# Kernel tuning notes

Hardware: AMD Instinct MI355X
Metric: run time of the kernel (lower is better)

## Reference

```python
import jax, jax.numpy as jnp
import numpy as np

D = 384; NH = 4; FF = 1024; NL = 2
L_ENC = 750; T_AUD = 1500; VOCAB = 60; T_TXT = 256; B = 8; S_SPK = 8; GAMA = 1.0


def _conv1d(x, w, b, stride):
    y = jax.lax.conv_general_dilated(x, w, (stride,), [(1, 1)], dimension_numbers=("NCH", "OIH", "NCH"))
    return y + b[None, :, None]


def _ln(x, g, b):
    m = x.mean(-1, keepdims=True)
    v = ((x - m) ** 2).mean(-1, keepdims=True)
    return (x - m) * jax.lax.rsqrt(v + 1e-5) * g + b


def _enc_layer(x, qkv_w, qkv_b, ow, ob, f1w, f1b, f2w, f2b, g1, b1, g2, b2):
    Bq, L, d = x.shape
    hd = d // NH
    q, k, v = jnp.split(x @ qkv_w.T + qkv_b, 3, axis=-1)
    q = q.reshape(Bq, L, NH, hd); k = k.reshape(Bq, L, NH, hd); v = v.reshape(Bq, L, NH, hd)
    s = jnp.einsum("blhd,bmhd->bhlm", q, k) * np.float32(1.0 / np.sqrt(hd))
    a = jax.nn.softmax(s, axis=-1)
    ctx = jnp.einsum("bhlm,bmhd->blhd", a, v).reshape(Bq, L, d)
    x = _ln(x + ctx @ ow.T + ob, g1, b1)
    h = jax.nn.relu(x @ f1w.T + f1b) @ f2w.T + f2b
    return _ln(x + h, g2, b2)


def _gru(x, h, wih, whh, bih, bhh):
    gi = x @ wih.T + bih
    gh = h @ whh.T + bhh
    ir, iz, inn = jnp.split(gi, 3, axis=-1)
    hr, hz, hn = jnp.split(gh, 3, axis=-1)
    r = jax.nn.sigmoid(ir + hr)
    z = jax.nn.sigmoid(iz + hz)
    n = jnp.tanh(inn + r * hn)
    return (1.0 - z) * n + z * h


def _nll(logits, tgt):
    # torch F.nll_loss applied to raw scores (faithful to source), ignore_index=-100
    valid = (tgt != -100)
    idx = jnp.where(valid, tgt, 0)
    picked = jnp.take_along_axis(logits, idx[..., None], axis=-1)[..., 0]
    return -(picked * valid).sum() / jnp.maximum(valid.sum(), 1).astype(logits.dtype)


def _forward(fl, target_asr_ids, target_diar_ids, remat=False):
    (input_features, speaker_inventory, conv1_w, conv1_b, conv2_w, conv2_b,
     asr_qkv_w, asr_qkv_b, asr_attn_out_w, asr_attn_out_b, asr_ff1_w, asr_ff1_b,
     asr_ff2_w, asr_ff2_b, asr_ln1_g, asr_ln1_b, asr_ln2_g, asr_ln2_b,
     diar_qkv_w, diar_qkv_b, diar_attn_out_w, diar_attn_out_b, diar_ff1_w, diar_ff1_b,
     diar_ff2_w, diar_ff2_b, diar_ln1_g, diar_ln1_b, diar_ln2_g, diar_ln2_b,
     la_q_w, la_k_w, la_v_w, la_in_b, la_out_w, la_out_b, emb,
     asr_rnn_w_ih, asr_rnn_w_hh, asr_rnn_b_ih, asr_rnn_b_hh,
     diar_rnn_w_ih, diar_rnn_w_hh, diar_rnn_b_ih, diar_rnn_b_hh,
     asr_out_w, asr_out_b, d2a_w, d2a_b, h2a_w, h2a_b) = fl
    x = jax.nn.relu(_conv1d(input_features, conv1_w, conv1_b, 1))
    x = jax.nn.relu(_conv1d(x, conv2_w, conv2_b, 2))
    x = jnp.transpose(x, (0, 2, 1))  # [B, L_ENC, D]
    enc_asr = x
    for l in range(NL):
        enc_asr = _enc_layer(enc_asr, asr_qkv_w[l], asr_qkv_b[l], asr_attn_out_w[l], asr_attn_out_b[l],
                             asr_ff1_w[l], asr_ff1_b[l], asr_ff2_w[l], asr_ff2_b[l],
                             asr_ln1_g[l], asr_ln1_b[l], asr_ln2_g[l], asr_ln2_b[l])
    enc_diar = x
    for l in range(NL):
        enc_diar = _enc_layer(enc_diar, diar_qkv_w[l], diar_qkv_b[l], diar_attn_out_w[l], diar_attn_out_b[l],
                              diar_ff1_w[l], diar_ff1_b[l], diar_ff2_w[l], diar_ff2_b[l],
                              diar_ln1_g[l], diar_ln1_b[l], diar_ln2_g[l], diar_ln2_b[l])
    Bsz = x.shape[0]
    inv_norm = jnp.linalg.norm(speaker_inventory, axis=2)  # [B, S]

    def step(carry, tgt):
        token, asr_ctx, h_asr, h_diar, attns = carry
        e = emb[token]  # [B, D]
        h_asr = _gru(jnp.concatenate([asr_ctx, e], 1), h_asr,
                     asr_rnn_w_ih, asr_rnn_w_hh, asr_rnn_b_ih, asr_rnn_b_hh)
        # 1-dim MultiheadAttention: q=h_asr[:,:,None], k=prev attentions, v=enc_asr (vdim=384->1)
        q = h_asr[:, :, None] * la_q_w[0, 0] + la_in_b[0]   # [B, L, 1]
        k = attns * la_k_w[0, 0] + la_in_b[1]               # [B, L, 1]
        v = enc_asr @ la_v_w.T + la_in_b[2]                 # [B, L, 1]
        s = q @ jnp.swapaxes(k, 1, 2)                       # [B, L, L]; head_dim=1 -> scale 1
        a = jax.nn.softmax(s, axis=-1)
        attns_new = (a @ v) * la_out_w[0, 0] + la_out_b[0]  # [B, L, 1]
        w = attns_new[..., 0]
        asr_ctx_new = jnp.einsum("bld,bl->bd", enc_asr, w)
        spk_ctx = jnp.einsum("bld,bl->bd", enc_diar, w)
        h_diar_new = _gru(jnp.concatenate([spk_ctx, e], 1), h_diar,
                          diar_rnn_w_ih, diar_rnn_w_hh, diar_rnn_b_ih, diar_rnn_b_hh)
        sc = jnp.einsum("bsd,bd->bs", speaker_inventory, h_diar_new)
        hn = jnp.linalg.norm(h_diar_new, axis=1, keepdims=True)
        beta = jax.nn.softmax(sc / (hn * inv_norm), axis=1)
        spk_state = jnp.einsum("bsd,bs->bd", speaker_inventory, beta)
        logits = (asr_ctx_new + h_asr @ h2a_w.T + h2a_b + spk_state @ d2a_w.T + d2a_b) @ asr_out_w.T + asr_out_b
        next_tok = jnp.where(tgt == -100, 0, tgt)
        return (next_tok, asr_ctx_new, h_asr, h_diar_new, attns_new), (logits, beta)

    step_fn = jax.checkpoint(step) if remat else step
    init = (jnp.zeros((Bsz,), jnp.int32),
            jnp.zeros((Bsz, D), jnp.float32),
            jnp.zeros((Bsz, L_ENC), jnp.float32),
            jnp.zeros((Bsz, D), jnp.float32),
            jnp.zeros((Bsz, L_ENC, 1), jnp.float32))
    _, (logits_seq, beta_seq) = jax.lax.scan(step_fn, init, jnp.swapaxes(target_asr_ids, 0, 1))
    asr_outputs = jnp.swapaxes(logits_seq, 0, 1)   # [B, T, VOCAB]
    diar_outputs = jnp.swapaxes(beta_seq, 0, 1)    # [B, T, S]
    loss = _nll(asr_outputs, target_asr_ids) + GAMA * _nll(diar_outputs, target_diar_ids)
    return asr_outputs, diar_outputs, loss


def setup_inputs() -> dict:
    key = jax.random.key(0)
    cnt = [0]
    def p(shape, scale=0.05):
        cnt[0] += 1
        return jax.random.normal(jax.random.fold_in(key, cnt[0]), shape, dtype=jnp.float32) * scale
    inp = {}
    inp["input_features"] = p((B, 80, T_AUD), 1.0)
    inp["speaker_inventory"] = p((B, S_SPK, D), 1.0)
    inp["conv1_w"] = p((D, 80, 3)); inp["conv1_b"] = p((D,))
    inp["conv2_w"] = p((D, D, 3)); inp["conv2_b"] = p((D,))
    for pre in ("asr", "diar"):
        inp[pre + "_qkv_w"] = p((NL, 3 * D, D)); inp[pre + "_qkv_b"] = p((NL, 3 * D))
        inp[pre + "_attn_out_w"] = p((NL, D, D)); inp[pre + "_attn_out_b"] = p((NL, D))
        inp[pre + "_ff1_w"] = p((NL, FF, D)); inp[pre + "_ff1_b"] = p((NL, FF))
        inp[pre + "_ff2_w"] = p((NL, D, FF)); inp[pre + "_ff2_b"] = p((NL, D))
        inp[pre + "_ln1_g"] = jnp.ones((NL, D), jnp.float32); inp[pre + "_ln1_b"] = jnp.zeros((NL, D), jnp.float32)
        inp[pre + "_ln2_g"] = jnp.ones((NL, D), jnp.float32); inp[pre + "_ln2_b"] = jnp.zeros((NL, D), jnp.float32)
    inp["la_q_w"] = p((1, 1), 1.0); inp["la_k_w"] = p((1, 1), 1.0); inp["la_v_w"] = p((1, D))
    inp["la_in_b"] = p((3,)); inp["la_out_w"] = p((1, 1), 1.0); inp["la_out_b"] = p((1,))
    inp["emb"] = p((VOCAB, D), 1.0)
    inp["asr_rnn_w_ih"] = p((3 * L_ENC, 2 * D)); inp["asr_rnn_w_hh"] = p((3 * L_ENC, L_ENC))
    inp["asr_rnn_b_ih"] = p((3 * L_ENC,)); inp["asr_rnn_b_hh"] = p((3 * L_ENC,))
    inp["diar_rnn_w_ih"] = p((3 * D, 2 * D)); inp["diar_rnn_w_hh"] = p((3 * D, D))
    inp["diar_rnn_b_ih"] = p((3 * D,)); inp["diar_rnn_b_hh"] = p((3 * D,))
    inp["asr_out_w"] = p((VOCAB, D)); inp["asr_out_b"] = p((VOCAB,))
    inp["d2a_w"] = p((D, D)); inp["d2a_b"] = p((D,))
    inp["h2a_w"] = p((D, L_ENC)); inp["h2a_b"] = p((D,))
    inp["target_asr_ids"] = jax.random.randint(jax.random.fold_in(key, 9001), (B, T_TXT), 0, VOCAB, dtype=jnp.int32)
    inp["target_diar_ids"] = jax.random.randint(jax.random.fold_in(key, 9002), (B, T_TXT), 0, S_SPK, dtype=jnp.int32)
    return inp


def reference(input_features, speaker_inventory, conv1_w, conv1_b, conv2_w, conv2_b,
              asr_qkv_w, asr_qkv_b, asr_attn_out_w, asr_attn_out_b, asr_ff1_w, asr_ff1_b,
              asr_ff2_w, asr_ff2_b, asr_ln1_g, asr_ln1_b, asr_ln2_g, asr_ln2_b,
              diar_qkv_w, diar_qkv_b, diar_attn_out_w, diar_attn_out_b, diar_ff1_w, diar_ff1_b,
              diar_ff2_w, diar_ff2_b, diar_ln1_g, diar_ln1_b, diar_ln2_g, diar_ln2_b,
              la_q_w, la_k_w, la_v_w, la_in_b, la_out_w, la_out_b, emb,
              asr_rnn_w_ih, asr_rnn_w_hh, asr_rnn_b_ih, asr_rnn_b_hh,
              diar_rnn_w_ih, diar_rnn_w_hh, diar_rnn_b_ih, diar_rnn_b_hh,
              asr_out_w, asr_out_b, d2a_w, d2a_b, h2a_w, h2a_b,
              target_asr_ids, target_diar_ids):
    fl = (input_features, speaker_inventory, conv1_w, conv1_b, conv2_w, conv2_b,
          asr_qkv_w, asr_qkv_b, asr_attn_out_w, asr_attn_out_b, asr_ff1_w, asr_ff1_b,
          asr_ff2_w, asr_ff2_b, asr_ln1_g, asr_ln1_b, asr_ln2_g, asr_ln2_b,
          diar_qkv_w, diar_qkv_b, diar_attn_out_w, diar_attn_out_b, diar_ff1_w, diar_ff1_b,
          diar_ff2_w, diar_ff2_b, diar_ln1_g, diar_ln1_b, diar_ln2_g, diar_ln2_b,
          la_q_w, la_k_w, la_v_w, la_in_b, la_out_w, la_out_b, emb,
          asr_rnn_w_ih, asr_rnn_w_hh, asr_rnn_b_ih, asr_rnn_b_hh,
          diar_rnn_w_ih, diar_rnn_w_hh, diar_rnn_b_ih, diar_rnn_b_hh,
          asr_out_w, asr_out_b, d2a_w, d2a_b, h2a_w, h2a_b)
    return _forward(fl, target_asr_ids, target_diar_ids, remat=False)
```

## Files before the change

kernel.cpp:

```cpp
#include <hip/hip_runtime.h>
#include <math.h>

#define L_ENC 750
#define T_AUD 1500
#define DD    384
#define FF    1024
#define NHH   4
#define HDIM  96
#define VOCAB 60
#define T_TXT 256
#define BB    8
#define NB    240
#define TB    512

static __device__ __forceinline__ float sigmf(float x){ return 1.f/(1.f + __expf(-x)); }

static __device__ __forceinline__ float cld(const float* p){
  return __hip_atomic_load(p, __ATOMIC_RELAXED, __HIP_MEMORY_SCOPE_AGENT);
}
static __device__ __forceinline__ void cst(float* p, float v){
  __hip_atomic_store(p, v, __ATOMIC_RELAXED, __HIP_MEMORY_SCOPE_AGENT);
}

static constexpr size_t O_X  = 0;
static constexpr size_t O_EA = 2304000;
static constexpr size_t O_ED = 4608000;
static constexpr size_t O_ST = 6912000;
static constexpr size_t oHASR = O_ST + 0;
static constexpr size_t oATT0 = O_ST + 6000;
static constexpr size_t oATT1 = O_ST + 12000;
static constexpr size_t oHD   = O_ST + 18000;
static constexpr size_t oACTX = O_ST + 21072;
static constexpr size_t oSCTX = O_ST + 27216;
static constexpr size_t oPREP = O_ST + 33360;
static constexpr size_t oGIA  = O_ST + 39504;
static constexpr size_t oGHA  = O_ST + 57504;
static constexpr size_t oGID  = O_ST + 75504;
static constexpr size_t oGHD  = O_ST + 84720;
static constexpr size_t oLACC = O_ST + 93936;
static constexpr size_t oVLA  = O_ST + 93944;
static constexpr size_t oINVN = O_ST + 99944;
static constexpr size_t oBAR  = O_ST + 100008;
static constexpr size_t oZ384 = O_ST + 102100;
static constexpr size_t O_SCR = O_ST + 103000;
static constexpr size_t oWIHAT_A = O_SCR + 0;
static constexpr size_t oWHHT_A  = O_SCR + 864000;
static constexpr size_t oWIHAT_D = O_SCR + 2556000;
static constexpr size_t oWHHT_D  = O_SCR + 2998368;
static constexpr size_t oH2AT    = O_SCR + 3440736;
static constexpr size_t oAOT     = O_SCR + 3728736;
static constexpr size_t oEMBT    = O_SCR + 3751776;
static constexpr size_t oGEA     = O_SCR + 4538208;
static constexpr size_t oGED     = O_SCR + 9146208;
static constexpr size_t oDIB     = O_SCR + 11505504;

__global__ void transpose_k(const float* __restrict__ in, int ldin, int R, int C,
                            float* __restrict__ out){
  __shared__ float t[32][33];
  int c0 = blockIdx.x*32, r0 = blockIdx.y*32;
  int x = threadIdx.x, y = threadIdx.y;
  for (int i = y; i < 32; i += 8){
    int r = r0 + i, c = c0 + x;
    t[i][x] = (r < R && c < C) ? in[(size_t)r*ldin + c] : 0.f;
  }
  __syncthreads();
  for (int i = y; i < 32; i += 8){
    int c = c0 + i, r = r0 + x;
    if (c < C && r < R) out[(size_t)c*R + r] = t[x][i];
  }
}

__global__ void packT_k(const float* __restrict__ in, int ldin, int R, int K,
                        float* __restrict__ out){
  __shared__ float tl[32][33];
  int k0 = blockIdx.x*32, r0 = blockIdx.y*32;
  int x = threadIdx.x, y = threadIdx.y;
  int K4 = ((K + 3) >> 2) << 2;
  for (int i = y; i < 32; i += 8){
    int r = r0 + i, k = k0 + x;
    tl[i][x] = (r < R && k < K) ? in[(size_t)r*ldin + k] : 0.f;
  }
  __syncthreads();
  for (int i = y; i < 32; i += 8){
    int k = k0 + i, r = r0 + x;
    if (k < K4 && r < R) out[((size_t)(k >> 2)*R + r)*4 + (k & 3)] = tl[x][i];
  }
}

__global__ void kt_k(const float* __restrict__ QKV, float* __restrict__ KT){
  __shared__ float t[32][33];
  int z = blockIdx.z; int b = z >> 2, h = z & 3;
  const float* in = QKV + (size_t)b*L_ENC*1152 + 384 + h*HDIM;
  float* out = KT + (size_t)z*HDIM*L_ENC;
  int c0 = blockIdx.x*32, r0 = blockIdx.y*32;
  int x = threadIdx.x, y = threadIdx.y;
  for (int i = y; i < 32; i += 8){
    int r = r0 + i, c = c0 + x;
    t[i][x] = (r < L_ENC && c < HDIM) ? in[(size_t)r*1152 + c] : 0.f;
  }
  __syncthreads();
  for (int i = y; i < 32; i += 8){
    int c = c0 + i, r = r0 + x;
    if (c < HDIM && r < L_ENC) out[(size_t)c*L_ENC + r] = t[x][i];
  }
}

template<int RELU, int HASRES>
__global__ __launch_bounds__(256) void gemm_k(
    const float* __restrict__ A, int lda, const float* __restrict__ W, int ldw,
    const float* __restrict__ bias, const float* __restrict__ Res,
    float* __restrict__ C, int ldc, int M, int N, int K)
{
  __shared__ __align__(16) float As[16][132];
  __shared__ __align__(16) float Ws[16][68];
  int tid = threadIdx.x;
  int row0 = blockIdx.y*128, col0 = blockIdx.x*64;
  int tx = tid & 15, ty = tid >> 4;
  int lr = tid >> 2, lk = (tid & 3)*4;
  float acc[8][4] = {};
  for (int k0 = 0; k0 < K; k0 += 16){
    float4 a0 = make_float4(0,0,0,0), a1 = make_float4(0,0,0,0), w0 = make_float4(0,0,0,0);
    int r0i = row0 + lr, r1i = row0 + 64 + lr, wri = col0 + lr;
    if (r0i < M) a0 = *(const float4*)(A + (size_t)r0i*lda + k0 + lk);
    if (r1i < M) a1 = *(const float4*)(A + (size_t)r1i*lda + k0 + lk);
    if (wri < N) w0 = *(const float4*)(W + (size_t)wri*ldw + k0 + lk);
    As[lk+0][lr] = a0.x; As[lk+1][lr] = a0.y; As[lk+2][lr] = a0.z; As[lk+3][lr] = a0.w;
    As[lk+0][64+lr] = a1.x; As[lk+1][64+lr] = a1.y; As[lk+2][64+lr] = a1.z; As[lk+3][64+lr] = a1.w;
    Ws[lk+0][lr] = w0.x; Ws[lk+1][lr] = w0.y; Ws[lk+2][lr] = w0.z; Ws[lk+3][lr] = w0.w;
    __syncthreads();
    #pragma unroll
    for (int k = 0; k < 16; k++){
      float4 b4 = *(const float4*)&Ws[k][tx*4];
      float4 a4 = *(const float4*)&As[k][ty*8];
      float4 a5 = *(const float4*)&As[k][ty*8+4];
      acc[0][0] += a4.x*b4.x; acc[0][1] += a4.x*b4.y; acc[0][2] += a4.x*b4.z; acc[0][3] += a4.x*b4.w;
      acc[1][0] += a4.y*b4.x; acc[1][1] += a4.y*b4.y; acc[1][2] += a4.y*b4.z; acc[1][3] += a4.y*b4.w;
      acc[2][0] += a4.z*b4.x; acc[2][1] += a4.z*b4.y; acc[2][2] += a4.z*b4.z; acc[2][3] += a4.z*b4.w;
      acc[3][0] += a4.w*b4.x; acc[3][1] += a4.w*b4.y; acc[3][2] += a4.w*b4.z; acc[3][3] += a4.w*b4.w;
      acc[4][0] += a5.x*b4.x; acc[4][1] += a5.x*b4.y; acc[4][2] += a5.x*b4.z; acc[4][3] += a5.x*b4.w;
      acc[5][0] += a5.y*b4.x; acc[5][1] += a5.y*b4.y; acc[5][2] += a5.y*b4.z; acc[5][3] += a5.y*b4.w;
      acc[6][0] += a5.z*b4.x; acc[6][1] += a5.z*b4.y; acc[6][2] += a5.z*b4.z; acc[6][3] += a5.z*b4.w;
      acc[7][0] += a5.w*b4.x; acc[7][1] += a5.w*b4.y; acc[7][2] += a5.w*b4.z; acc[7][3] += a5.w*b4.w;
    }
    __syncthreads();
  }
  #pragma unroll
  for (int ii = 0; ii < 8; ii++){
    int m = row0 + ty*8 + ii;
    if (m >= M) continue;
    #pragma unroll
    for (int jj = 0; jj < 4; jj++){
      int n = col0 + tx*4 + jj;
      if (n >= N) continue;
      float v = acc[ii][jj] + bias[n];
      if (HASRES) v += Res[(size_t)m*ldc + n];
      if (RELU) v = fmaxf(v, 0.f);
      C[(size_t)m*ldc + n] = v;
    }
  }
}

__global__ void im2col1(const float* __restrict__ in, float* __restrict__ P){
  int t = blockIdx.x, b = blockIdx.y, i = threadIdx.x;
  if (i >= 240) return;
  int ic = i/3, kt = i - ic*3;
  int p = t + kt - 1;
  P[((size_t)(b*T_AUD + t))*240 + i] = (p >= 0 && p < T_AUD) ? in[((size_t)(b*80 + ic))*T_AUD + p] : 0.f;
}

__global__ __launch_bounds__(384) void im2col2(const float* __restrict__ X1T, float* __restrict__ P){
  int t = blockIdx.x, b = blockIdx.y, ic = threadIdx.x;
  size_t ob = ((size_t)(b*L_ENC + t))*1152 + (size_t)ic*3;
  #pragma unroll
  for (int kt = 0; kt < 3; kt++){
    int p = 2*t + kt - 1;
    P[ob + kt] = (p >= 0 && p < T_AUD) ? X1T[((size_t)(b*T_AUD + p))*DD + ic] : 0.f;
  }
}

__global__ __launch_bounds__(256) void dup_k(const float* __restrict__ src,
    float* __restrict__ a, float* __restrict__ b){
  size_t i = (size_t)blockIdx.x*256 + threadIdx.x;
  float4 v = ((const float4*)src)[i];
  ((float4*)a)[i] = v;
  ((float4*)b)[i] = v;
}

__global__ __launch_bounds__(128) void ln_k(float* __restrict__ X, const float* __restrict__ g,
                                            const float* __restrict__ bt){
  int r = blockIdx.x, tid = threadIdx.x;
  float* p = X + (size_t)r*DD;
  float v0 = p[tid], v1 = p[tid+128], v2 = p[tid+256];
  __shared__ float red[128];
  red[tid] = v0+v1+v2; __syncthreads();
  for (int k = 64; k > 0; k >>= 1){ if (tid < k) red[tid] += red[tid+k]; __syncthreads(); }
  float m = red[0] * (1.f/384.f);
  __syncthreads();
  float d0 = v0-m, d1 = v1-m, d2 = v2-m;
  red[tid] = d0*d0 + d1*d1 + d2*d2; __syncthreads();
  for (int k = 64; k > 0; k >>= 1){ if (tid < k) red[tid] += red[tid+k]; __syncthreads(); }
  float rs = rsqrtf(red[0]*(1.f/384.f) + 1e-5f);
  p[tid]     = d0*rs*g[tid]     + bt[tid];
  p[tid+128] = d1*rs*g[tid+128] + bt[tid+128];
  p[tid+256] = d2*rs*g[tid+256] + bt[tid+256];
}

__global__ __launch_bounds__(1024) void attn_enc(const float* __restrict__ QKV,
    const float* __restrict__ KT, float* __restrict__ ctx){
  int b = blockIdx.z, h = blockIdx.y, i0 = blockIdx.x*16;
  int tid = threadIdx.x, lane = tid & 63, wv = tid >> 6;
  __shared__ float q_s[16][96];
  __shared__ float p_s[16][752];
  __shared__ float den_s[16];
  for (int idx = tid; idx < 16*96; idx += 1024){
    int r2 = idx/96, c = idx - r2*96; int i = i0 + r2;
    q_s[r2][c] = (i < L_ENC) ? QKV[((size_t)(b*L_ENC + i))*1152 + h*HDIM + c]*0.10206207f : 0.f;
  }
  __syncthreads();
  int i = i0 + wv;
  const float* ktb = KT + ((size_t)(b*4 + h))*HDIM*L_ENC;
  if (i < L_ENC){
    float sr[12] = {0,0,0,0,0,0,0,0,0,0,0,0};
    for (int c = 0; c < 96; c++){
      float qc = q_s[wv][c];
      const float* kr = ktb + c*L_ENC + lane;
      #pragma unroll
      for (int jt = 0; jt < 12; jt++) sr[jt] += qc*kr[jt*64];
    }
    float mx = -1e30f;
    #pragma unroll
    for (int jt = 0; jt < 12; jt++){ if (lane + jt*64 < L_ENC) mx = fmaxf(mx, sr[jt]); }
    #pragma unroll
    for (int o = 32; o > 0; o >>= 1) mx = fmaxf(mx, __shfl_xor(mx, o));
    float den = 0.f;
    #pragma unroll
    for (int jt = 0; jt < 12; jt++){
      int j = lane + jt*64;
      if (j < L_ENC){ float e = __expf(sr[jt]-mx); p_s[wv][j] = e; den += e; }
    }
    #pragma unroll
    for (int o = 32; o > 0; o >>= 1) den += __shfl_xor(den, o);
    if (lane == 0) den_s[wv] = den;
  }
  __syncthreads();
  if (i < L_ENC){
    float idn = 1.f/den_s[wv];
    const float* vb = QKV + (size_t)b*L_ENC*1152 + 768 + h*HDIM;
    float a0 = 0.f, a1 = 0.f;
    for (int j = 0; j < L_ENC; j++){
      float pj = p_s[wv][j];
      const float* vr = vb + (size_t)j*1152;
      a0 += pj*vr[lane];
      if (lane < 32) a1 += pj*vr[lane + 64];
    }
    size_t ob = ((size_t)(b*L_ENC + i))*DD + h*HDIM;
    ctx[ob + lane] = a0*idn;
    if (lane < 32) ctx[ob + lane + 64] = a1*idn;
  }
}

__global__ __launch_bounds__(384) void embed_k(const float* __restrict__ emb,
    const int* __restrict__ tgtA, float* __restrict__ E){
  int row = blockIdx.x; int t = row >> 3, b = row & 7;
  int tok = 0;
  if (t > 0){ int v = tgtA[b*T_TXT + t - 1]; tok = (v == -100) ? 0 : v; }
  E[(size_t)row*DD + threadIdx.x] = emb[(size_t)tok*DD + threadIdx.x];
}

__global__ __launch_bounds__(256) void vla_k(const float* __restrict__ EA,
    const float* __restrict__ lav, const float* __restrict__ lain, float* __restrict__ VLA){
  int row = blockIdx.x*4 + (threadIdx.x >> 6);
  int lane = threadIdx.x & 63;
  if (row >= BB*L_ENC) return;
  const float* p = EA + (size_t)row*DD;
  float s = 0.f;
  for (int d = lane; d < DD; d += 64) s += p[d]*lav[d];
  #pragma unroll
  for (int o = 32; o > 0; o >>= 1) s += __shfl_xor(s, o);
  if (lane == 0) VLA[row] = s + lain[2];
}

__global__ void invn_k(const float* __restrict__ inv, float* __restrict__ INVN){
  int row = blockIdx.x; int lane = threadIdx.x;
  float s = 0.f;
  for (int d = lane; d < DD; d += 64){ float v = inv[(size_t)row*DD + d]; s += v*v; }
  #pragma unroll
  for (int o = 32; o > 0; o >>= 1) s += __shfl_xor(s, o);
  if (lane == 0) INVN[row] = sqrtf(s);
}

struct DecParams {
  float* ws; float* out;
  const float* ABHH; const float* DBHH;
  const float* SPK;  const float* AOB;
  const float* LAQ; const float* LAK; const float* LAIB; const float* LAOW; const float* LAOB;
  const float* H2AB; const float* D2AB;
  const int* TGTA; const int* TGTD;
};

static __device__ __forceinline__ void gbar(unsigned* s, unsigned epoch){
  __syncthreads();
  int tid = threadIdx.x;
  if (blockIdx.x == 0){
    if (tid > 0 && tid < NB){
      while (__hip_atomic_load(&s[tid*4], __ATOMIC_RELAXED, __HIP_MEMORY_SCOPE_AGENT) < epoch)
        __builtin_amdgcn_s_sleep(4);
    }
    __syncthreads();
    if (tid < NB)
      __hip_atomic_store(&s[(256 + tid)*4], epoch, __ATOMIC_RELAXED, __HIP_MEMORY_SCOPE_AGENT);
  } else {
    if (tid == 0){
      __hip_atomic_store(&s[blockIdx.x*4], epoch, __ATOMIC_RELAXED, __HIP_MEMORY_SCOPE_AGENT);
      while (__hip_atomic_load(&s[(256 + blockIdx.x)*4], __ATOMIC_RELAXED, __HIP_MEMORY_SCOPE_AGENT) < epoch)
        __builtin_amdgcn_s_sleep(4);
    }
    __syncthreads();
  }
}

#define FMA8(acc, s_, base) { const float4 b0_ = *(const float4*)&(base)[0]; const float4 b1_ = *(const float4*)&(base)[4]; \
  acc[0]+=b0_.x*(s_); acc[1]+=b0_.y*(s_); acc[2]+=b0_.z*(s_); acc[3]+=b0_.w*(s_); \
  acc[4]+=b1_.x*(s_); acc[5]+=b1_.y*(s_); acc[6]+=b1_.z*(s_); acc[7]+=b1_.w*(s_); }

template<int NR, int KH, int KQH>
__device__ void gates_fn(int task, const float* __restrict__ WIT, const float* __restrict__ WHT,
                         const float* __restrict__ ctxv, const float* __restrict__ hv,
                         const float* __restrict__ GE, const float* __restrict__ bhh,
                         float* __restrict__ GI, float* __restrict__ GH, int t, float* SM)
{
  constexpr int CHQ = (KQH + 31) / 32;
  float* ac  = SM;
  float* hh  = SM + 3072;
  float* pgi = SM + 3072 + KQH*32;
  float* pgh = pgi + 4096;
  int tid = threadIdx.x;
  for (int idx = tid; idx < 3072; idx += TB){ int b = idx/384, k = idx - b*384; ac[k*8+b] = cld(&ctxv[idx]); }
  for (int idx = tid; idx < KH*8;  idx += TB){ int b = idx/KH,  k = idx - b*KH;  hh[k*8+b] = cld(&hv[idx]); }
  for (int idx = KH*8 + tid; idx < KQH*32; idx += TB) hh[idx] = 0.f;
  __syncthreads();
  int rl = tid & 15, kp = tid >> 4;
  int r = task*16 + rl;
  float gi[8] = {}, gh[8] = {};
  if (r < NR){
    const float4* W4 = (const float4*)WIT;
    int q0 = kp*3;
    #pragma unroll
    for (int q = q0; q < q0+3; q++){
      float4 w4 = W4[(size_t)q*NR + r];
      const float* a = &ac[q*32];
      FMA8(gi, w4.x, a+0); FMA8(gi, w4.y, a+8); FMA8(gi, w4.z, a+16); FMA8(gi, w4.w, a+24);
    }
    const float4* WH4 = (const float4*)WHT;
    int h0 = kp*CHQ, h1 = (h0 + CHQ < KQH) ? h0 + CHQ : KQH;
    for (int q = h0; q < h1; q++){
      float4 w4 = WH4[(size_t)q*NR + r];
      const float* a = &hh[q*32];
      FMA8(gh, w4.x, a+0); FMA8(gh, w4.y, a+8); FMA8(gh, w4.z, a+16); FMA8(gh, w4.w, a+24);
    }
  }
  #pragma unroll
  for (int b = 0; b < 8; b++){ pgi[(kp*16+rl)*8 + b] = gi[b]; pgh[(kp*16+rl)*8 + b] = gh[b]; }
  __syncthreads();
  if (tid < 16){
    int rr = task*16 + tid;
    if (rr < NR){
      #pragma unroll
      for (int b = 0; b < 8; b++){
        float s1 = 0.f, s2 = 0.f;
        for (int kq = 0; kq < 32; kq++){ s1 += pgi[(kq*16+tid)*8 + b]; s2 += pgh[(kq*16+tid)*8 + b]; }
        cst(&GI[(size_t)b*NR + rr], s1 + GE[((size_t)t*8 + b)*NR + rr]);
        cst(&GH[(size_t)b*NR + rr], s2 + bhh[rr]);
      }
    }
  }
  __syncthreads();
}

__device__ void phase_hattn_ctx(int bid, int t, float* ws, const DecParams& P, float* SM)
{
  float* kk = SM;
  float* vv = SM + 768;
  float* wl = SM + 1536;
  float* hl = SM + 1568;
  float* part = SM + 1600;
  int tid = threadIdx.x;
  int b = bid & 7, chunk = bid >> 3;
  int i0 = chunk*26; int n = L_ENC - i0; if (n > 26) n = 26;
  const float* acur = ws + ((t & 1) ? oATT1 : oATT0);
  float*       anxt = ws + ((t & 1) ? oATT0 : oATT1);
  const float* GIAp = ws + oGIA; const float* GHAp = ws + oGHA;
  float* HASRp = ws + oHASR;
  const float* VLAp = ws + oVLA;
  float kw = P.LAK[0], kb = P.LAIB[1];
  for (int j = tid; j < L_ENC; j += TB){
    kk[j] = cld(&acur[b*L_ENC + j])*kw + kb;
    vv[j] = VLAp[b*L_ENC + j];
  }
  __syncthreads();
  int wv = tid >> 6, lane = tid & 63;
  float laq = P.LAQ[0], li0 = P.LAIB[0], low = P.LAOW[0], lob = P.LAOB[0];
  for (int il = wv; il < n; il += 8){
    int i = i0 + il;
    int base = b*2250 + i;
    float rr = sigmf(cld(&GIAp[base]) + cld(&GHAp[base]));
    float zz = sigmf(cld(&GIAp[base+750]) + cld(&GHAp[base+750]));
    float nn = tanhf(cld(&GIAp[base+1500]) + rr*cld(&GHAp[base+1500]));
    float h = (1.f - zz)*nn + zz*cld(&HASRp[b*L_ENC + i]);
    float q = h*laq + li0;
    float sr[12]; float mx = -1e30f;
    #pragma unroll
    for (int jt = 0; jt < 12; jt++){
      int j = lane + jt*64;
      float s = (j < L_ENC) ? q*kk[j] : -1e30f;
      sr[jt] = s; mx = fmaxf(mx, s);
    }
    #pragma unroll
    for (int o = 32; o > 0; o >>= 1) mx = fmaxf(mx, __shfl_xor(mx, o));
    float se = 0.f, sv = 0.f;
    #pragma unroll
    for (int jt = 0; jt < 12; jt++){
      int j = lane + jt*64;
      if (j < L_ENC){ float e = __expf(sr[jt] - mx); se += e; sv += e*vv[j]; }
    }
    #pragma unroll
    for (int o = 32; o > 0; o >>= 1){ se += __shfl_xor(se, o); sv += __shfl_xor(sv, o); }
    if (lane == 0){
      cst(&HASRp[b*L_ENC + i], h);
      float w = (sv/se)*low + lob;
      cst(&anxt[b*L_ENC + i], w);
      wl[il] = w; hl[il] = h;
    }
  }
  __syncthreads();
  if (tid < 480){
    int lg = tid / 96, dq = tid - lg*96;
    int d0 = dq*4;
    const float* EAb = ws + O_EA + (size_t)b*L_ENC*DD + d0;
    const float* EDb = ws + O_ED + (size_t)b*L_ENC*DD + d0;
    const float* H2b = ws + oH2AT + d0;
    float4 a4 = {0,0,0,0}, s4 = {0,0,0,0}, h4 = {0,0,0,0};
    for (int j = lg; j < n; j += 5){
      size_t lo = (size_t)(i0 + j)*DD;
      float wj = wl[j], hj = hl[j];
      float4 e = *(const float4*)(EAb + lo);
      a4.x += e.x*wj; a4.y += e.y*wj; a4.z += e.z*wj; a4.w += e.w*wj;
      float4 e2 = *(const float4*)(EDb + lo);
      s4.x += e2.x*wj; s4.y += e2.y*wj; s4.z += e2.z*wj; s4.w += e2.w*wj;
      float4 e3 = *(const float4*)(H2b + lo);
      h4.x += e3.x*hj; h4.y += e3.y*hj; h4.z += e3.z*hj; h4.w += e3.w*hj;
    }
    float* pp = part + (size_t)tid*12;
    *(float4*)pp = a4; *(float4*)(pp+4) = s4; *(float4*)(pp+8) = h4;
  }
  __syncthreads();
  if (tid < 96){
    float4 ra = {0,0,0,0}, rs = {0,0,0,0}, rh = {0,0,0,0};
    #pragma unroll
    for (int g = 0; g < 5; g++){
      const float* pp = part + (size_t)(g*96 + tid)*12;
      float4 pa = *(const float4*)pp, ps = *(const float4*)(pp+4), ph = *(const float4*)(pp+8);
      ra.x += pa.x; ra.y += pa.y; ra.z += pa.z; ra.w += pa.w;
      rs.x += ps.x; rs.y += ps.y; rs.z += ps.z; rs.w += ps.w;
      rh.x += ph.x; rh.y += ph.y; rh.z += ph.z; rh.w += ph.w;
    }
    int par = t & 1;
    int d0 = tid*4;
    float* A = &ws[oACTX + par*3072 + b*DD + d0];
    float* S = &ws[oSCTX + par*3072 + b*DD + d0];
    float* Pr = &ws[oPREP + par*3072 + b*DD + d0];
    atomicAdd(&A[0], ra.x); atomicAdd(&A[1], ra.y); atomicAdd(&A[2], ra.z); atomicAdd(&A[3], ra.w);
    atomicAdd(&S[0], rs.x); atomicAdd(&S[1], rs.y); atomicAdd(&S[2], rs.z); atomicAdd(&S[3], rs.w);
    atomicAdd(&Pr[0], ra.x+rh.x); atomicAdd(&Pr[1], ra.y+rh.y);
    atomicAdd(&Pr[2], ra.z+rh.z); atomicAdd(&Pr[3], ra.w+rh.w);
  }
  __syncthreads();
}

__device__ void phase_final(int b, int t, float* ws, const float* prep,
                            const DecParams& P, float* SM)
{
  float* hd_s = SM;
  float* pre_s = SM + 384;
  float* red = SM + 768;
  float* beta_s = SM + 1280;
  float* sc_s = SM + 1288;
  float* part2 = SM + 1296;
  int tid = threadIdx.x;
  bool act = tid < DD;
  const float* GIDp = ws + oGID; const float* GHDp = ws + oGHD;
  float* HDp = ws + oHD;
  float h = 0.f;
  if (act){
    int base = b*1152 + tid;
    float rr = sigmf(cld(&GIDp[base]) + cld(&GHDp[base]));
    float zz = sigmf(cld(&GIDp[base+384]) + cld(&GHDp[base+384]));
    float nn = tanhf(cld(&GIDp[base+768]) + rr*cld(&GHDp[base+768]));
    h = (1.f - zz)*nn + zz*cld(&HDp[b*DD + tid]);
    hd_s[tid] = h; cst(&HDp[b*DD + tid], h);
  }
  red[tid] = act ? h*h : 0.f;
  __syncthreads();
  for (int s = 256; s > 0; s >>= 1){ if (tid < s) red[tid] += red[tid+s]; __syncthreads(); }
  float hn = sqrtf(red[0]);
  int sg = tid >> 6, lane = tid & 63;
  float ps = 0.f;
  for (int j = lane; j < DD; j += 64) ps += P.SPK[((size_t)(b*8 + sg))*DD + j]*hd_s[j];
  #pragma unroll
  for (int o = 32; o > 0; o >>= 1) ps += __shfl_xor(ps, o);
  if (lane == 0) sc_s[sg] = ps / (hn * ws[oINVN + b*8 + sg]);
  __syncthreads();
  if (tid == 0){
    float mx = -1e30f;
    for (int s2 = 0; s2 < 8; s2++) mx = fmaxf(mx, sc_s[s2]);
    float sm = 0.f;
    for (int s2 = 0; s2 < 8; s2++){ float e = __expf(sc_s[s2] - mx); beta_s[s2] = e; sm += e; }
    float isv = 1.f/sm;
    for (int s2 = 0; s2 < 8; s2++) beta_s[s2] *= isv;
    int td = P.TGTD[b*T_TXT + t];
    if (td != -100){ atomicAdd(&ws[oLACC+2], beta_s[td]); atomicAdd(&ws[oLACC+3], 1.f); }
  }
  __syncthreads();
  if (tid < 8) P.out[122880 + ((size_t)(b*T_TXT + t))*8 + tid] = beta_s[tid];
  if (act){
    float p = cld(&prep[b*DD + tid]);
    const float* Mb = ws + oDIB + (size_t)(b*8)*DD + tid;
    #pragma unroll
    for (int s2 = 0; s2 < 8; s2++) p += beta_s[s2]*Mb[(size_t)s2*DD];
    pre_s[tid] = p;
  }
  __syncthreads();
  {
    int vg = tid >> 6, v = tid & 63;
    float pl = 0.f;
    if (v < VOCAB){
      const float* AOTp = ws + oAOT;
      int d0 = vg*48;
      for (int d2 = d0; d2 < d0+48; d2++) pl += pre_s[d2]*AOTp[d2*VOCAB + v];
    }
    part2[vg*64 + v] = pl;
  }
  __syncthreads();
  if (tid < VOCAB){
    float lg = P.AOB[tid];
    #pragma unroll
    for (int g = 0; g < 8; g++) lg += part2[g*64 + tid];
    P.out[((size_t)(b*T_TXT + t))*VOCAB + tid] = lg;
    int ta = P.TGTA[b*T_TXT + t];
    if (ta == tid) atomicAdd(&ws[oLACC+0], lg);
    if (tid == 0 && ta != -100) atomicAdd(&ws[oLACC+1], 1.f);
  }
  __syncthreads();
}

__global__ __launch_bounds__(TB) void dec_loop(DecParams P)
{
  __shared__ __align__(16) float SM[17280];
  int bid = blockIdx.x;
  float* ws = P.ws;
  unsigned* slots = (unsigned*)(ws + oBAR);
  unsigned ep = 0;

  if (bid < 141)
    gates_fn<2250,750,188>(bid, ws+oWIHAT_A, ws+oWHHT_A, ws+oACTX, ws+oHASR,
                           ws+oGEA, P.ABHH, ws+oGIA, ws+oGHA, 0, SM);
  else if (bid < 149){
    int b = bid - 141;
    for (int d = threadIdx.x; d < DD; d += TB)
      cst(&ws[oPREP + b*DD + d], P.H2AB[d] + P.D2AB[d]);
  }
  gbar(slots, ++ep);

  for (int t = 0; t <= T_TXT; t++){
    if (t < T_TXT && bid < 232) phase_hattn_ctx(bid, t, ws, P, SM);
    else if (bid >= 232 && t >= 1)
      phase_final(bid - 232, t - 1, ws, ws + oPREP + ((t-1) & 1)*3072, P, SM);
    gbar(slots, ++ep);
    if (t == T_TXT) break;

    if (bid < 72)
      gates_fn<1152,384,96>(bid, ws+oWIHAT_D, ws+oWHHT_D, ws+oSCTX+(t&1)*3072, ws+oHD,
                            ws+oGED, P.DBHH, ws+oGID, ws+oGHD, t, SM);
    else if (bid < 213){
      if (t + 1 < T_TXT)
        gates_fn<2250,750,188>(bid-72, ws+oWIHAT_A, ws+oWHHT_A, ws+oACTX+(t&1)*3072, ws+oHASR,
                               ws+oGEA, P.ABHH, ws+oGIA, ws+oGHA, t+1, SM);
    } else if (bid < 221 && t + 1 < T_TXT){
      int b = bid - 213, par = (t + 1) & 1;
      for (int d = threadIdx.x; d < DD; d += TB){
        cst(&ws[oACTX + par*3072 + b*DD + d], 0.f);
        cst(&ws[oSCTX + par*3072 + b*DD + d], 0.f);
        cst(&ws[oPREP + par*3072 + b*DD + d], P.H2AB[d] + P.D2AB[d]);
      }
    }
    gbar(slots, ++ep);
  }
}

__global__ void loss_final_k(const float* __restrict__ lacc, float* __restrict__ out){
  if (threadIdx.x == 0 && blockIdx.x == 0){
    float la = lacc[0]/fmaxf(lacc[1], 1.f);
    float ld = lacc[2]/fmaxf(lacc[3], 1.f);
    out[139264] = -(la + ld);
  }
}

extern "C" void kernel_launch(void* const* d_in, const int* in_sizes, int n_in,
                              void* d_out, int out_size, void* d_ws, size_t ws_size,
                              hipStream_t stream)
{
  (void)in_sizes; (void)n_in; (void)out_size; (void)ws_size;
  float* ws  = (float*)d_ws;
  float* out = (float*)d_out;

  const float* IN0   = (const float*)d_in[0];
  const float* SPK   = (const float*)d_in[1];
  const float* C1W   = (const float*)d_in[2];
  const float* C1B   = (const float*)d_in[3];
  const float* C2W   = (const float*)d_in[4];
  const float* C2B   = (const float*)d_in[5];
  const float* LAQ   = (const float*)d_in[30];
  const float* LAK   = (const float*)d_in[31];
  const float* LAV   = (const float*)d_in[32];
  const float* LAIB  = (const float*)d_in[33];
  const float* LAOW  = (const float*)d_in[34];
  const float* LAOB  = (const float*)d_in[35];
  const float* EMB   = (const float*)d_in[36];
  const float* AWIH  = (const float*)d_in[37];
  const float* AWHH  = (const float*)d_in[38];
  const float* ABIH  = (const float*)d_in[39];
  const float* ABHH  = (const float*)d_in[40];
  const float* DWIH  = (const float*)d_in[41];
  const float* DWHH  = (const float*)d_in[42];
  const float* DBIH  = (const float*)d_in[43];
  const float* DBHH  = (const float*)d_in[44];
  const float* AOW   = (const float*)d_in[45];
  const float* AOB   = (const float*)d_in[46];
  const float* D2AW  = (const float*)d_in[47];
  const float* D2AB  = (const float*)d_in[48];
  const float* H2AW  = (const float*)d_in[49];
  const float* H2AB  = (const float*)d_in[50];
  const int*   TGTA  = (const int*)d_in[51];
  const int*   TGTD  = (const int*)d_in[52];

  const size_t S_QKV = O_SCR;
  const size_t S_KT  = O_SCR + 6912000;
  const size_t S_CTX = O_SCR + 9216000;
  const size_t S_Y   = O_SCR + 11520000;
  const size_t S_H   = O_SCR + 13824000;
  const size_t X1T   = S_KT;
  const size_t Pc1   = S_H;
  const size_t Pc2   = S_QKV;

  hipMemsetAsync((void*)(ws + O_ST), 0, 103000*sizeof(float), stream);

  im2col1<<<dim3(1500,8), 256, 0, stream>>>(IN0, ws + Pc1);
  gemm_k<1,0><<<dim3(6,94), 256, 0, stream>>>(ws+Pc1, 240, C1W, 240, C1B, nullptr, ws+X1T, 384, 12000, 384, 240);
  im2col2<<<dim3(750,8), 384, 0, stream>>>(ws+X1T, ws+Pc2);
  gemm_k<1,0><<<dim3(6,47), 256, 0, stream>>>(ws+Pc2, 1152, C2W, 1152, C2B, nullptr, ws+O_X, 384, 6000, 384, 1152);

  dup_k<<<2250, 256, 0, stream>>>(ws+O_X, ws+O_EA, ws+O_ED);

  auto enc_layer = [&](float* Xb, const float* qw, const float* qb, const float* ow,
                       const float* ob, const float* f1w, const float* f1b,
                       const float* f2w, const float* f2b,
                       const float* g1, const float* b1, const float* g2, const float* b2){
    gemm_k<0,0><<<dim3(18,47), 256, 0, stream>>>(Xb, 384, qw, 384, qb, nullptr, ws+S_QKV, 1152, 6000, 1152, 384);
    kt_k<<<dim3(3,24,32), dim3(32,8), 0, stream>>>(ws+S_QKV, ws+S_KT);
    attn_enc<<<dim3(47,4,8), 1024, 0, stream>>>(ws+S_QKV, ws+S_KT, ws+S_CTX);
    gemm_k<0,1><<<dim3(6,47), 256, 0, stream>>>(ws+S_CTX, 384, ow, 384, ob, Xb, ws+S_Y, 384, 6000, 384, 384);
    ln_k<<<6000, 128, 0, stream>>>(ws+S_Y, g1, b1);
    gemm_k<1,0><<<dim3(16,47), 256, 0, stream>>>(ws+S_Y, 384, f1w, 384, f1b, nullptr, ws+S_H, 1024, 6000, 1024, 384);
    gemm_k<0,1><<<dim3(6,47), 256, 0, stream>>>(ws+S_H, 1024, f2w, 1024, f2b, ws+S_Y, Xb, 384, 6000, 384, 1024);
    ln_k<<<6000, 128, 0, stream>>>(Xb, g2, b2);
  };
  for (int st = 0; st < 2; st++){
    int base = (st == 0) ? 6 : 18;
    float* Xb = ws + ((st == 0) ? O_EA : O_ED);
    const float* qkvw = (const float*)d_in[base+0];
    const float* qkvb = (const float*)d_in[base+1];
    const float* aow  = (const float*)d_in[base+2];
    const float* aob2 = (const float*)d_in[base+3];
    const float* f1w  = (const float*)d_in[base+4];
    const float* f1b  = (const float*)d_in[base+5];
    const float* f2w  = (const float*)d_in[base+6];
    const float* f2b  = (const float*)d_in[base+7];
    const float* g1   = (const float*)d_in[base+8];
    const float* b1   = (const float*)d_in[base+9];
    const float* g2   = (const float*)d_in[base+10];
    const float* b2   = (const float*)d_in[base+11];
    for (int l = 0; l < 2; l++){
      enc_layer(Xb, qkvw + (size_t)l*1152*384, qkvb + (size_t)l*1152,
                aow + (size_t)l*384*384, aob2 + (size_t)l*384,
                f1w + (size_t)l*1024*384, f1b + (size_t)l*1024,
                f2w + (size_t)l*384*1024, f2b + (size_t)l*384,
                g1 + (size_t)l*384, b1 + (size_t)l*384, g2 + (size_t)l*384, b2 + (size_t)l*384);
    }
  }

  packT_k<<<dim3(12,71), dim3(32,8), 0, stream>>>(AWIH, 768, 2250, 384, ws+oWIHAT_A);
  packT_k<<<dim3(24,71), dim3(32,8), 0, stream>>>(AWHH, 750, 2250, 750, ws+oWHHT_A);
  packT_k<<<dim3(12,36), dim3(32,8), 0, stream>>>(DWIH, 768, 1152, 384, ws+oWIHAT_D);
  packT_k<<<dim3(12,36), dim3(32,8), 0, stream>>>(DWHH, 384, 1152, 384, ws+oWHHT_D);
  transpose_k<<<dim3(24,12), dim3(32,8), 0, stream>>>(H2AW, 750, 384, 750, ws+oH2AT);
  transpose_k<<<dim3(12,2),  dim3(32,8), 0, stream>>>(AOW, 384, 60, 384, ws+oAOT);
  embed_k<<<2048, 384, 0, stream>>>(EMB, TGTA, ws+oEMBT);
  gemm_k<0,0><<<dim3(36,16), 256, 0, stream>>>(ws+oEMBT, 384, AWIH+384, 768, ABIH, nullptr, ws+oGEA, 2250, 2048, 2250, 384);
  gemm_k<0,0><<<dim3(18,16), 256, 0, stream>>>(ws+oEMBT, 384, DWIH+384, 768, DBIH, nullptr, ws+oGED, 1152, 2048, 1152, 384);
  gemm_k<0,0><<<dim3(6,1), 256, 0, stream>>>(SPK, 384, D2AW, 384, ws+oZ384, nullptr, ws+oDIB, 384, 64, 384, 384);
  vla_k<<<1500, 256, 0, stream>>>(ws+O_EA, LAV, LAIB, ws+oVLA);
  invn_k<<<64, 64, 0, stream>>>(SPK, ws+oINVN);

  DecParams DP;
  DP.ws = ws; DP.out = out;
  DP.ABHH = ABHH; DP.DBHH = DBHH; DP.SPK = SPK; DP.AOB = AOB;
  DP.LAQ = LAQ; DP.LAK = LAK; DP.LAIB = LAIB; DP.LAOW = LAOW; DP.LAOB = LAOB;
  DP.H2AB = H2AB; DP.D2AB = D2AB; DP.TGTA = TGTA; DP.TGTD = TGTD;
  dec_loop<<<dim3(NB), dim3(TB), 0, stream>>>(DP);

  loss_final_k<<<1, 64, 0, stream>>>(ws+oLACC, out);
}
```

Before: 20.64 ms.

## Widen GEMM tiles, double decoder grid, parallelize gate reduction

The GEMM kernel now computes 128x128 output tiles with an 8x8 register micro-tile per thread instead of 128x64, halving grid width in every launch and raising arithmetic intensity per shared-memory load. The persistent decoder loop grows from 240 to 480 blocks, with barrier slots and scratch offsets shifted to match, and the gate-partial reduction now splits across 128 threads (row x batch) instead of 16. The GEMM change doubles accumulator registers, which may cut occupancy. Using more decoder blocks spreads the gate matvec K-range thinner but makes each grid barrier more expensive.

```diff
diff --git a/kernel.cpp b/kernel.cpp
--- a/kernel.cpp
+++ b/kernel.cpp
@@ -10,7 +10,7 @@
 #define VOCAB 60
 #define T_TXT 256
 #define BB    8
-#define NB    240
+#define NB    480
 #define TB    512
 
 static __device__ __forceinline__ float sigmf(float x){ return 1.f/(1.f + __expf(-x)); }
@@ -41,8 +41,8 @@
 static constexpr size_t oVLA  = O_ST + 93944;
 static constexpr size_t oINVN = O_ST + 99944;
 static constexpr size_t oBAR  = O_ST + 100008;
-static constexpr size_t oZ384 = O_ST + 102100;
-static constexpr size_t O_SCR = O_ST + 103000;
+static constexpr size_t oZ384 = O_ST + 104200;
+static constexpr size_t O_SCR = O_ST + 105000;
 static constexpr size_t oWIHAT_A = O_SCR + 0;
 static constexpr size_t oWHHT_A  = O_SCR + 864000;
 static constexpr size_t oWIHAT_D = O_SCR + 2556000;
@@ -112,45 +112,51 @@
     float* __restrict__ C, int ldc, int M, int N, int K)
 {
   __shared__ __align__(16) float As[16][132];
-  __shared__ __align__(16) float Ws[16][68];
+  __shared__ __align__(16) float Ws[16][132];
   int tid = threadIdx.x;
-  int row0 = blockIdx.y*128, col0 = blockIdx.x*64;
+  int row0 = blockIdx.y*128, col0 = blockIdx.x*128;
   int tx = tid & 15, ty = tid >> 4;
-  int lr = tid >> 2, lk = (tid & 3)*4;
-  float acc[8][4] = {};
+  int lr = tid >> 1, lk = (tid & 1)*8;
+  float acc[8][8] = {};
+  int ar = row0 + lr, wr = col0 + lr;
   for (int k0 = 0; k0 < K; k0 += 16){
-    float4 a0 = make_float4(0,0,0,0), a1 = make_float4(0,0,0,0), w0 = make_float4(0,0,0,0);
-    int r0i = row0 + lr, r1i = row0 + 64 + lr, wri = col0 + lr;
-    if (r0i < M) a0 = *(const float4*)(A + (size_t)r0i*lda + k0 + lk);
-    if (r1i < M) a1 = *(const float4*)(A + (size_t)r1i*lda + k0 + lk);
-    if (wri < N) w0 = *(const float4*)(W + (size_t)wri*ldw + k0 + lk);
+    float4 a0 = make_float4(0,0,0,0), a1 = make_float4(0,0,0,0);
+    float4 w0 = make_float4(0,0,0,0), w1 = make_float4(0,0,0,0);
+    if (ar < M){
+      const float* ap = A + (size_t)ar*lda + k0 + lk;
+      a0 = *(const float4*)ap; a1 = *(const float4*)(ap + 4);
+    }
+    if (wr < N){
+      const float* wp = W + (size_t)wr*ldw + k0 + lk;
+      w0 = *(const float4*)wp; w1 = *(const float4*)(wp + 4);
+    }
+    __syncthreads();
     As[lk+0][lr] = a0.x; As[lk+1][lr] = a0.y; As[lk+2][lr] = a0.z; As[lk+3][lr] = a0.w;
-    As[lk+0][64+lr] = a1.x; As[lk+1][64+lr] = a1.y; As[lk+2][64+lr] = a1.z; As[lk+3][64+lr] = a1.w;
+    As[lk+4][lr] = a1.x; As[lk+5][lr] = a1.y; As[lk+6][lr] = a1.z; As[lk+7][lr] = a1.w;
     Ws[lk+0][lr] = w0.x; Ws[lk+1][lr] = w0.y; Ws[lk+2][lr] = w0.z; Ws[lk+3][lr] = w0.w;
+    Ws[lk+4][lr] = w1.x; Ws[lk+5][lr] = w1.y; Ws[lk+6][lr] = w1.z; Ws[lk+7][lr] = w1.w;
     __syncthreads();
     #pragma unroll
     for (int k = 0; k < 16; k++){
-      float4 b4 = *(const float4*)&Ws[k][tx*4];
-      float4 a4 = *(const float4*)&As[k][ty*8];
-      float4 a5 = *(const float4*)&As[k][ty*8+4];
-      acc[0][0] += a4.x*b4.x; acc[0][1] += a4.x*b4.y; acc[0][2] += a4.x*b4.z; acc[0][3] += a4.x*b4.w;
-      acc[1][0] += a4.y*b4.x; acc[1][1] += a4.y*b4.y; acc[1][2] += a4.y*b4.z; acc[1][3] += a4.y*b4.w;
-      acc[2][0] += a4.z*b4.x; acc[2][1] += a4.z*b4.y; acc[2][2] += a4.z*b4.z; acc[2][3] += a4.z*b4.w;
-      acc[3][0] += a4.w*b4.x; acc[3][1] += a4.w*b4.y; acc[3][2] += a4.w*b4.z; acc[3][3] += a4.w*b4.w;
-      acc[4][0] += a5.x*b4.x; acc[4][1] += a5.x*b4.y; acc[4][2] += a5.x*b4.z; acc[4][3] += a5.x*b4.w;
-      acc[5][0] += a5.y*b4.x; acc[5][1] += a5.y*b4.y; acc[5][2] += a5.y*b4.z; acc[5][3] += a5.y*b4.w;
-      acc[6][0] += a5.z*b4.x; acc[6][1] += a5.z*b4.y; acc[6][2] += a5.z*b4.z; acc[6][3] += a5.z*b4.w;
-      acc[7][0] += a5.w*b4.x; acc[7][1] += a5.w*b4.y; acc[7][2] += a5.w*b4.z; acc[7][3] += a5.w*b4.w;
-    }
-    __syncthreads();
+      float av[8], bv[8];
+      *(float4*)&av[0] = *(const float4*)&As[k][ty*8];
+      *(float4*)&av[4] = *(const float4*)&As[k][ty*8+4];
+      *(float4*)&bv[0] = *(const float4*)&Ws[k][tx*8];
+      *(float4*)&bv[4] = *(const float4*)&Ws[k][tx*8+4];
+      #pragma unroll
+      for (int ii = 0; ii < 8; ii++){
+        #pragma unroll
+        for (int jj = 0; jj < 8; jj++) acc[ii][jj] += av[ii]*bv[jj];
+      }
+    }
   }
   #pragma unroll
   for (int ii = 0; ii < 8; ii++){
     int m = row0 + ty*8 + ii;
     if (m >= M) continue;
     #pragma unroll
-    for (int jj = 0; jj < 4; jj++){
-      int n = col0 + tx*4 + jj;
+    for (int jj = 0; jj < 8; jj++){
+      int n = col0 + tx*8 + jj;
       if (n >= N) continue;
       float v = acc[ii][jj] + bias[n];
       if (HASRES) v += Res[(size_t)m*ldc + n];
@@ -308,11 +314,11 @@
     }
     __syncthreads();
     if (tid < NB)
-      __hip_atomic_store(&s[(256 + tid)*4], epoch, __ATOMIC_RELAXED, __HIP_MEMORY_SCOPE_AGENT);
+      __hip_atomic_store(&s[(512 + tid)*4], epoch, __ATOMIC_RELAXED, __HIP_MEMORY_SCOPE_AGENT);
   } else {
     if (tid == 0){
       __hip_atomic_store(&s[blockIdx.x*4], epoch, __ATOMIC_RELAXED, __HIP_MEMORY_SCOPE_AGENT);
-      while (__hip_atomic_load(&s[(256 + blockIdx.x)*4], __ATOMIC_RELAXED, __HIP_MEMORY_SCOPE_AGENT) < epoch)
+      while (__hip_atomic_load(&s[(512 + blockIdx.x)*4], __ATOMIC_RELAXED, __HIP_MEMORY_SCOPE_AGENT) < epoch)
         __builtin_amdgcn_s_sleep(4);
     }
     __syncthreads();
@@ -329,7 +335,6 @@
                          const float* __restrict__ GE, const float* __restrict__ bhh,
                          float* __restrict__ GI, float* __restrict__ GH, int t, float* SM)
 {
-  constexpr int CHQ = (KQH + 31) / 32;
   float* ac  = SM;
   float* hh  = SM + 3072;
   float* pgi = SM + 3072 + KQH*32;
@@ -344,15 +349,14 @@
   float gi[8] = {}, gh[8] = {};
   if (r < NR){
     const float4* W4 = (const float4*)WIT;
-    int q0 = kp*3;
-    #pragma unroll
-    for (int q = q0; q < q0+3; q++){
+    int q0 = (kp*96) >> 5, q1 = ((kp+1)*96) >> 5;
+    for (int q = q0; q < q1; q++){
       float4 w4 = W4[(size_t)q*NR + r];
       const float* a = &ac[q*32];
       FMA8(gi, w4.x, a+0); FMA8(gi, w4.y, a+8); FMA8(gi, w4.z, a+16); FMA8(gi, w4.w, a+24);
     }
     const float4* WH4 = (const float4*)WHT;
-    int h0 = kp*CHQ, h1 = (h0 + CHQ < KQH) ? h0 + CHQ : KQH;
+    int h0 = (kp*KQH) >> 5, h1 = ((kp+1)*KQH) >> 5;
     for (int q = h0; q < h1; q++){
       float4 w4 = WH4[(size_t)q*NR + r];
       const float* a = &hh[q*32];
@@ -362,16 +366,15 @@
   #pragma unroll
   for (int b = 0; b < 8; b++){ pgi[(kp*16+rl)*8 + b] = gi[b]; pgh[(kp*16+rl)*8 + b] = gh[b]; }
   __syncthreads();
-  if (tid < 16){
-    int rr = task*16 + tid;
+  if (tid < 128){
+    int rl2 = tid & 15, bb = tid >> 4;
+    int rr = task*16 + rl2;
     if (rr < NR){
+      float s1 = 0.f, s2 = 0.f;
       #pragma unroll
-      for (int b = 0; b < 8; b++){
-        float s1 = 0.f, s2 = 0.f;
-        for (int kq = 0; kq < 32; kq++){ s1 += pgi[(kq*16+tid)*8 + b]; s2 += pgh[(kq*16+tid)*8 + b]; }
-        cst(&GI[(size_t)b*NR + rr], s1 + GE[((size_t)t*8 + b)*NR + rr]);
-        cst(&GH[(size_t)b*NR + rr], s2 + bhh[rr]);
-      }
+      for (int kq = 0; kq < 32; kq++){ s1 += pgi[(kq*16+rl2)*8+bb]; s2 += pgh[(kq*16+rl2)*8+bb]; }
+      cst(&GI[(size_t)bb*NR + rr], s1 + GE[((size_t)t*8 + bb)*NR + rr]);
+      cst(&GH[(size_t)bb*NR + rr], s2 + bhh[rr]);
     }
   }
   __syncthreads();
@@ -553,7 +556,7 @@
   __syncthreads();
 }
 
-__global__ __launch_bounds__(TB) void dec_loop(DecParams P)
+__global__ __launch_bounds__(TB, 4) void dec_loop(DecParams P)
 {
   __shared__ __align__(16) float SM[17280];
   int bid = blockIdx.x;
@@ -573,7 +576,7 @@
 
   for (int t = 0; t <= T_TXT; t++){
     if (t < T_TXT && bid < 232) phase_hattn_ctx(bid, t, ws, P, SM);
-    else if (bid >= 232 && t >= 1)
+    else if (bid >= 232 && bid < 240 && t >= 1)
       phase_final(bid - 232, t - 1, ws, ws + oPREP + ((t-1) & 1)*3072, P, SM);
     gbar(slots, ++ep);
     if (t == T_TXT) break;
@@ -652,12 +655,12 @@
   const size_t Pc1   = S_H;
   const size_t Pc2   = S_QKV;
 
-  hipMemsetAsync((void*)(ws + O_ST), 0, 103000*sizeof(float), stream);
+  hipMemsetAsync((void*)(ws + O_ST), 0, 105000*sizeof(float), stream);
 
   im2col1<<<dim3(1500,8), 256, 0, stream>>>(IN0, ws + Pc1);
-  gemm_k<1,0><<<dim3(6,94), 256, 0, stream>>>(ws+Pc1, 240, C1W, 240, C1B, nullptr, ws+X1T, 384, 12000, 384, 240);
+  gemm_k<1,0><<<dim3(3,94), 256, 0, stream>>>(ws+Pc1, 240, C1W, 240, C1B, nullptr, ws+X1T, 384, 12000, 384, 240);
   im2col2<<<dim3(750,8), 384, 0, stream>>>(ws+X1T, ws+Pc2);
-  gemm_k<1,0><<<dim3(6,47), 256, 0, stream>>>(ws+Pc2, 1152, C2W, 1152, C2B, nullptr, ws+O_X, 384, 6000, 384, 1152);
+  gemm_k<1,0><<<dim3(3,47), 256, 0, stream>>>(ws+Pc2, 1152, C2W, 1152, C2B, nullptr, ws+O_X, 384, 6000, 384, 1152);
 
   dup_k<<<2250, 256, 0, stream>>>(ws+O_X, ws+O_EA, ws+O_ED);
 
@@ -665,13 +668,13 @@
                        const float* ob, const float* f1w, const float* f1b,
                        const float* f2w, const float* f2b,
                        const float* g1, const float* b1, const float* g2, const float* b2){
-    gemm_k<0,0><<<dim3(18,47), 256, 0, stream>>>(Xb, 384, qw, 384, qb, nullptr, ws+S_QKV, 1152, 6000, 1152, 384);
+    gemm_k<0,0><<<dim3(9,47), 256, 0, stream>>>(Xb, 384, qw, 384, qb, nullptr, ws+S_QKV, 1152, 6000, 1152, 384);
     kt_k<<<dim3(3,24,32), dim3(32,8), 0, stream>>>(ws+S_QKV, ws+S_KT);
     attn_enc<<<dim3(47,4,8), 1024, 0, stream>>>(ws+S_QKV, ws+S_KT, ws+S_CTX);
-    gemm_k<0,1><<<dim3(6,47), 256, 0, stream>>>(ws+S_CTX, 384, ow, 384, ob, Xb, ws+S_Y, 384, 6000, 384, 384);
+    gemm_k<0,1><<<dim3(3,47), 256, 0, stream>>>(ws+S_CTX, 384, ow, 384, ob, Xb, ws+S_Y, 384, 6000, 384, 384);
     ln_k<<<6000, 128, 0, stream>>>(ws+S_Y, g1, b1);
-    gemm_k<1,0><<<dim3(16,47), 256, 0, stream>>>(ws+S_Y, 384, f1w, 384, f1b, nullptr, ws+S_H, 1024, 6000, 1024, 384);
-    gemm_k<0,1><<<dim3(6,47), 256, 0, stream>>>(ws+S_H, 1024, f2w, 1024, f2b, ws+S_Y, Xb, 384, 6000, 384, 1024);
+    gemm_k<1,0><<<dim3(8,47), 256, 0, stream>>>(ws+S_Y, 384, f1w, 384, f1b, nullptr, ws+S_H, 1024, 6000, 1024, 384);
+    gemm_k<0,1><<<dim3(3,47), 256, 0, stream>>>(ws+S_H, 1024, f2w, 1024, f2b, ws+S_Y, Xb, 384, 6000, 384, 1024);
     ln_k<<<6000, 128, 0, stream>>>(Xb, g2, b2);
   };
   for (int st = 0; st < 2; st++){
@@ -705,9 +708,9 @@
   transpose_k<<<dim3(24,12), dim3(32,8), 0, stream>>>(H2AW, 750, 384, 750, ws+oH2AT);
   transpose_k<<<dim3(12,2),  dim3(32,8), 0, stream>>>(AOW, 384, 60, 384, ws+oAOT);
   embed_k<<<2048, 384, 0, stream>>>(EMB, TGTA, ws+oEMBT);
-  gemm_k<0,0><<<dim3(36,16), 256, 0, stream>>>(ws+oEMBT, 384, AWIH+384, 768, ABIH, nullptr, ws+oGEA, 2250, 2048, 2250, 384);
-  gemm_k<0,0><<<dim3(18,16), 256, 0, stream>>>(ws+oEMBT, 384, DWIH+384, 768, DBIH, nullptr, ws+oGED, 1152, 2048, 1152, 384);
-  gemm_k<0,0><<<dim3(6,1), 256, 0, stream>>>(SPK, 384, D2AW, 384, ws+oZ384, nullptr, ws+oDIB, 384, 64, 384, 384);
+  gemm_k<0,0><<<dim3(18,16), 256, 0, stream>>>(ws+oEMBT, 384, AWIH+384, 768, ABIH, nullptr, ws+oGEA, 2250, 2048, 2250, 384);
+  gemm_k<0,0><<<dim3(9,16), 256, 0, stream>>>(ws+oEMBT, 384, DWIH+384, 768, DBIH, nullptr, ws+oGED, 1152, 2048, 1152, 384);
+  gemm_k<0,0><<<dim3(3,1), 256, 0, stream>>>(SPK, 384, D2AW, 384, ws+oZ384, nullptr, ws+oDIB, 384, 64, 384, 384);
   vla_k<<<1500, 256, 0, stream>>>(ws+O_EA, LAV, LAIB, ws+oVLA);
   invn_k<<<64, 64, 0, stream>>>(SPK, ws+oINVN);
 
```

New measurement: 20.62 ms. About the same (-0.1%).
